# Kernel optimization log

Measured on AMD Instinct MI355X. Metric: run time of the kernel, lower is better.

Reference implementation:

```python
import jax, jax.numpy as jnp
import numpy as np

B, S, D = 30, 1024, 128      # batch (hardcoded by module), seq_len, input_dim
ET, H, NH = 128, 4, 128      # embed_time, num_heads, nhidden
DK = ET // H


def setup_inputs() -> dict:
    key = jax.random.key(0)
    ks = jax.random.split(key, 32)
    s = 0.05
    p = lambda i, shape: jax.random.normal(ks[i], shape, jnp.float32) * s
    return dict(
        x=jax.random.normal(ks[0], (B, S, D), jnp.float32),
        time_steps=jax.random.uniform(ks[1], (B, S), jnp.float32),
        # learned time embedding: Linear(1,1) and Linear(1, ET-1)
        w_lin=p(2, (1, 1)), b_lin=p(3, (1,)),
        w_per=p(4, (ET - 1, 1)), b_per=p(5, (ET - 1,)),
        # attention projections
        Wq=p(6, (ET, ET)), bq=p(7, (ET,)),
        Wk=p(8, (ET, ET)), bk=p(9, (ET,)),
        Wo=p(10, (NH, D * H)), bo=p(11, (NH,)),
        # bidirectional GRU (forward / backward directions)
        Wih_f=p(12, (3 * NH, NH)), Whh_f=p(13, (3 * NH, NH)),
        bih_f=p(14, (3 * NH,)), bhh_f=p(15, (3 * NH,)),
        Wih_b=p(16, (3 * NH, NH)), Whh_b=p(17, (3 * NH, NH)),
        bih_b=p(18, (3 * NH,)), bhh_b=p(19, (3 * NH,)),
        # classifier (no activations in original Sequential)
        W1=p(20, (128, 2 * NH)), b1=p(21, (128,)),
        W2=p(22, (64, 128)), b2=p(23, (64,)),
        W3=p(24, (6, 64)), b3=p(25, (6,)),
    )


def _gru_final(xseq, Wih, Whh, bih, bhh):
    # xseq: [S, B, NH]; returns final hidden [B, NH] (PyTorch GRU equations)
    def step(h, xt):
        gi = xt @ Wih.T + bih
        gh = h @ Whh.T + bhh
        ir, iz, inn = jnp.split(gi, 3, axis=-1)
        hr, hz, hn = jnp.split(gh, 3, axis=-1)
        r = jax.nn.sigmoid(ir + hr)
        z = jax.nn.sigmoid(iz + hz)
        n = jnp.tanh(inn + r * hn)
        h_new = (1.0 - z) * n + z * h
        return h_new, None
    h0 = jnp.zeros((xseq.shape[1], Whh.shape[1]), xseq.dtype)
    hT, _ = jax.lax.scan(step, h0, xseq)
    return hT


def reference(x, time_steps, w_lin, b_lin, w_per, b_per, Wq, bq, Wk, bk, Wo, bo,
              Wih_f, Whh_f, bih_f, bhh_f, Wih_b, Whh_b, bih_b, bhh_b,
              W1, b1, W2, b2, W3, b3):
    # learned time embedding: cat([Linear(1,1)(t), sin(Linear(1,ET-1)(t))], -1)
    tt = time_steps[..., None]                                   # [B,S,1]
    te = jnp.concatenate([tt @ w_lin.T + b_lin,
                          jnp.sin(tt @ w_per.T + b_per)], -1)    # [B,S,ET]
    # q/k projections, split into heads
    q = (te @ Wq.T + bq).reshape(B, S, H, DK).transpose(0, 2, 1, 3)  # [B,H,S,DK]
    k = (te @ Wk.T + bk).reshape(B, S, H, DK).transpose(0, 2, 1, 3)
    scores = jnp.einsum('bhqd,bhkd->bhqk', q, k) / jnp.sqrt(jnp.float32(DK))
    # mask=None, dropout=None => the repeat_interleave over the feature dim is
    # redundant: softmax over the key axis is identical for every feature, so
    # sum(p_attn * value) == softmax(scores) @ value exactly.
    attn = jax.nn.softmax(scores, axis=-1)                       # [B,H,S,S]
    ctx = jnp.einsum('bhqk,bkd->bhqd', attn, x)                  # [B,H,S,D]
    att_out = ctx.transpose(0, 2, 1, 3).reshape(B, S, H * D) @ Wo.T + bo  # [B,S,NH]
    # bidirectional GRU; only final hidden states are used downstream
    xs = att_out.transpose(1, 0, 2)                              # [S,B,NH]
    hf = _gru_final(xs, Wih_f, Whh_f, bih_f, bhh_f)
    hb = _gru_final(xs[::-1], Wih_b, Whh_b, bih_b, bhh_b)
    cin = jnp.concatenate([hf, hb], axis=-1)                     # [B,2*NH]
    h1 = cin @ W1.T + b1
    h2 = h1 @ W2.T + b2
    return h2 @ W3.T + b3                                        # [B,6]
```

## Files before the change

### kernel.cpp

```cpp
#include <hip/hip_runtime.h>
#include <math.h>

#define B_ 30
#define S_ 1024
#define D_ 128
#define ET_ 128
#define H_ 4
#define DK_ 32
#define NH_ 128
#define NPOS (B_*S_)

#define OFF_TE   0L
#define OFF_Q    3932160L
#define OFF_K    7864320L
#define OFF_CTX  11796480L
#define OFF_XS   0L
#define OFF_GIF  3932160L
#define OFF_GIB  15728640L
#define OFF_HF   27525120L
#define OFF_HB   27528960L

typedef __attribute__((ext_vector_type(4))) short short4v;
typedef __attribute__((ext_vector_type(8))) short short8v;
typedef __attribute__((ext_vector_type(4))) float f32x4;

__device__ __forceinline__ short f2bf(float x) {
    unsigned u = __builtin_bit_cast(unsigned, x);
    unsigned r = (u + 0x7FFFu + ((u >> 16) & 1u)) >> 16;
    return (short)r;
}
__device__ __forceinline__ float bf2f(short s) {
    unsigned u = ((unsigned)(unsigned short)s) << 16;
    return __builtin_bit_cast(float, u);
}

__device__ __forceinline__ short8v pack8(const float4 a, const float4 b) {
    short8v v;
    v[0]=f2bf(a.x); v[1]=f2bf(a.y); v[2]=f2bf(a.z); v[3]=f2bf(a.w);
    v[4]=f2bf(b.x); v[5]=f2bf(b.y); v[6]=f2bf(b.z); v[7]=f2bf(b.w);
    return v;
}

__device__ __forceinline__ void pack_hilo(const float4 a, const float4 b,
                                          short8v& hi, short8v& lo) {
    float v[8] = {a.x,a.y,a.z,a.w,b.x,b.y,b.z,b.w};
#pragma unroll
    for (int e = 0; e < 8; ++e) {
        hi[e] = f2bf(v[e]);
        lo[e] = f2bf(v[e] - bf2f(hi[e]));
    }
}

__device__ __forceinline__ float fsigmoid(float x) {
    return 1.f / (1.f + __expf(-x));
}
__device__ __forceinline__ float ftanh(float x) {
    return 1.f - 2.f / (__expf(2.f * x) + 1.f);
}

__device__ __forceinline__ void sync_lds() {
    asm volatile("s_waitcnt lgkmcnt(0)" ::: "memory");
    __builtin_amdgcn_sched_barrier(0);
    __builtin_amdgcn_s_barrier();
    __builtin_amdgcn_sched_barrier(0);
}

__global__ __launch_bounds__(256) void time_embed_kernel(
    const float* __restrict__ ts, const float* __restrict__ w_lin,
    const float* __restrict__ b_lin, const float* __restrict__ w_per,
    const float* __restrict__ b_per, float* __restrict__ te)
{
    const long idx = (long)blockIdx.x * 256 + threadIdx.x;
    const int pos = (int)(idx >> 7);
    const int j = (int)(idx & 127);
    const float tv = ts[pos];
    float v;
    if (j == 0) v = tv * w_lin[0] + b_lin[0];
    else        v = sinf(tv * w_per[j-1] + b_per[j-1]);
    te[idx] = v;
}

template<int REMAP, int FOLD>
__global__ __launch_bounds__(256) void gemm_mfma_kernel(
    const float* __restrict__ A, const float* __restrict__ W,
    const float* __restrict__ bias, const float* __restrict__ bias2,
    float* __restrict__ C, int M, int N, int K)
{
    __shared__ short A_hi[64][72], A_lo[64][72];
    __shared__ short W_hi[128][72], W_lo[128][72];
    const int t = threadIdx.x;
    const int m0 = blockIdx.x * 64;
    const int n0 = blockIdx.y * 128;
    const int w = t >> 6, lane = t & 63;
    const int l15 = lane & 15, lg = lane >> 4;

    f32x4 acc[8];
#pragma unroll
    for (int i = 0; i < 8; ++i) acc[i] = (f32x4){0.f,0.f,0.f,0.f};

    for (int k0 = 0; k0 < K; k0 += 64) {
        {
            const int r = t >> 2, c16 = (t & 3) * 16;
            const int m = m0 + r;
            long src;
            if (REMAP == 2) {
                const int s = m / B_, bb = m % B_;
                src = (long)((S_-1-s)*B_ + bb) * K;
            } else {
                src = (long)m * K;
            }
            const float4* ap = (const float4*)(A + src + k0 + c16);
            short8v h0, l0, h1, l1;
            pack_hilo(ap[0], ap[1], h0, l0);
            pack_hilo(ap[2], ap[3], h1, l1);
            *(short8v*)&A_hi[r][c16]     = h0;
            *(short8v*)&A_hi[r][c16 + 8] = h1;
            *(short8v*)&A_lo[r][c16]     = l0;
            *(short8v*)&A_lo[r][c16 + 8] = l1;
        }
        {
            const int n = t >> 1, c32 = (t & 1) * 32;
            const float4* wp = (const float4*)(W + (long)(n0 + n) * K + k0 + c32);
#pragma unroll
            for (int q = 0; q < 4; ++q) {
                short8v h, l;
                pack_hilo(wp[2*q], wp[2*q + 1], h, l);
                *(short8v*)&W_hi[n][c32 + 8*q] = h;
                *(short8v*)&W_lo[n][c32 + 8*q] = l;
            }
        }
        __syncthreads();
#pragma unroll
        for (int kk = 0; kk < 64; kk += 32) {
            short8v ah = *(const short8v*)&A_hi[16*w + l15][kk + 8*lg];
            short8v al = *(const short8v*)&A_lo[16*w + l15][kk + 8*lg];
#pragma unroll
            for (int nf = 0; nf < 8; ++nf) {
                short8v wh = *(const short8v*)&W_hi[16*nf + l15][kk + 8*lg];
                short8v wl = *(const short8v*)&W_lo[16*nf + l15][kk + 8*lg];
                acc[nf] = __builtin_amdgcn_mfma_f32_16x16x32_bf16(ah, wh, acc[nf], 0,0,0);
                acc[nf] = __builtin_amdgcn_mfma_f32_16x16x32_bf16(al, wh, acc[nf], 0,0,0);
                acc[nf] = __builtin_amdgcn_mfma_f32_16x16x32_bf16(ah, wl, acc[nf], 0,0,0);
            }
        }
        __syncthreads();
    }

#pragma unroll
    for (int nf = 0; nf < 8; ++nf) {
#pragma unroll
        for (int r = 0; r < 4; ++r) {
            const int n = n0 + 16*nf + l15;
            const int m = m0 + 16*w + 4*lg + r;
            float v = acc[nf][r] + bias[n];
            if (FOLD) { if (n < 256) v += bias2[n]; }
            if (REMAP == 1) {
                const int bb = m / S_, s = m % S_;
                C[(long)(s*B_ + bb) * N + n] = v;
            } else {
                C[(long)m * N + n] = v;
            }
        }
    }
}

#define SCALE_LOG2 (0.17677669529663687f * 1.4426950408889634f)

__global__ __launch_bounds__(256) void attn_kernel(
    const float* __restrict__ qbuf, const float* __restrict__ kbuf,
    const float* __restrict__ x, float* __restrict__ ctx)
{
    const int qt = blockIdx.x;
    const int h  = blockIdx.y;
    const int b  = blockIdx.z;
    const int q0 = qt * 64;
    const int t  = threadIdx.x;
    const int w    = t >> 6;
    const int lane = t & 63;
    const int l15  = lane & 15;
    const int lg   = lane >> 4;

    __shared__ short K_lds[64][40];
    __shared__ short XT_lds[128][68];
    __shared__ short P_lds[4][16][88];

    short8v qf;
    {
        const float* qp = qbuf + ((long)(b*S_ + q0 + 16*w + l15))*ET_ + h*DK_ + 8*lg;
        float4 a = *(const float4*)qp;
        float4 c = *(const float4*)(qp + 4);
        a.x*=SCALE_LOG2; a.y*=SCALE_LOG2; a.z*=SCALE_LOG2; a.w*=SCALE_LOG2;
        c.x*=SCALE_LOG2; c.y*=SCALE_LOG2; c.z*=SCALE_LOG2; c.w*=SCALE_LOG2;
        qf = pack8(a, c);
    }

    short8v ones;
#pragma unroll
    for (int i = 0; i < 8; ++i) ones[i] = (short)0x3F80;

    f32x4 acc[8];
#pragma unroll
    for (int i = 0; i < 8; ++i) acc[i] = (f32x4){0.f,0.f,0.f,0.f};
    float lsum = 0.f;
    const f32x4 zf = (f32x4){0.f,0.f,0.f,0.f};

    for (int kt = 0; kt < 16; ++kt) {
        const int key0 = kt * 64;
        {
            const int key = t >> 2, c8 = (t & 3) * 8;
            const float* kp = kbuf + ((long)(b*S_ + key0 + key))*ET_ + h*DK_ + c8;
            float4 a = *(const float4*)kp;
            float4 c = *(const float4*)(kp + 4);
            *(short8v*)&K_lds[key][c8] = pack8(a, c);
        }
        {
            const int k2 = t & 31;
            const int dg = t >> 5;
            const float* xp0 = x + ((long)(b*S_ + key0 + 2*k2))*D_ + 16*dg;
            const float* xp1 = xp0 + D_;
            float v0[16], v1[16];
#pragma unroll
            for (int j4 = 0; j4 < 4; ++j4) {
                float4 a = ((const float4*)xp0)[j4];
                float4 c = ((const float4*)xp1)[j4];
                v0[4*j4+0]=a.x; v0[4*j4+1]=a.y; v0[4*j4+2]=a.z; v0[4*j4+3]=a.w;
                v1[4*j4+0]=c.x; v1[4*j4+1]=c.y; v1[4*j4+2]=c.z; v1[4*j4+3]=c.w;
            }
#pragma unroll
            for (int j = 0; j < 16; ++j) {
                unsigned u = (unsigned)(unsigned short)f2bf(v0[j])
                           | ((unsigned)(unsigned short)f2bf(v1[j]) << 16);
                *(unsigned*)&XT_lds[16*dg + j][2*k2] = u;
            }
        }
        __syncthreads();

        f32x4 sc[4];
#pragma unroll
        for (int f = 0; f < 4; ++f) {
            short8v kf = *(const short8v*)&K_lds[16*f + l15][8*lg];
            sc[f] = __builtin_amdgcn_mfma_f32_16x16x32_bf16(kf, qf, zf, 0, 0, 0);
        }

        float pw[4][4];
        float ps = 0.f;
#pragma unroll
        for (int f = 0; f < 4; ++f)
#pragma unroll
            for (int r = 0; r < 4; ++r) {
                const float p = exp2f(sc[f][r]);
                ps += p;
                pw[f][r] = p - 1.f;
            }
        ps += __shfl_xor(ps, 16);
        ps += __shfl_xor(ps, 32);
        lsum += ps;

#pragma unroll
        for (int f = 0; f < 4; ++f) {
            unsigned lo = (unsigned)(unsigned short)f2bf(pw[f][0])
                        | ((unsigned)(unsigned short)f2bf(pw[f][1]) << 16);
            unsigned hi = (unsigned)(unsigned short)f2bf(pw[f][2])
                        | ((unsigned)(unsigned short)f2bf(pw[f][3]) << 16);
            *(unsigned*)&P_lds[w][l15][16*f + 4*lg]     = lo;
            *(unsigned*)&P_lds[w][l15][16*f + 4*lg + 2] = hi;
        }

#pragma unroll
        for (int kb = 0; kb < 2; ++kb) {
            short8v pa = *(const short8v*)&P_lds[w][l15][32*kb + 8*lg];
#pragma unroll
            for (int dq = 0; dq < 8; ++dq) {
                const short* xr = &XT_lds[16*dq + l15][32*kb + 8*lg];
                short4v lo = *(const short4v*)xr;
                short4v hi = *(const short4v*)(xr + 4);
                short8v xb = __builtin_shufflevector(lo, hi, 0,1,2,3,4,5,6,7);
                acc[dq] = __builtin_amdgcn_mfma_f32_16x16x32_bf16(ones, xb, acc[dq], 0, 0, 0);
                acc[dq] = __builtin_amdgcn_mfma_f32_16x16x32_bf16(pa,   xb, acc[dq], 0, 0, 0);
            }
        }
        __syncthreads();
    }

    const float inv = 1.f / lsum;
#pragma unroll
    for (int r = 0; r < 4; ++r) {
        const float ir = __shfl(inv, (lane & 48) | (4*lg + r));
        const long base = ((long)(b*S_ + q0 + 16*w + 4*lg + r)*H_ + h)*D_ + l15;
#pragma unroll
        for (int d = 0; d < 8; ++d)
            ctx[base + (long)d*16] = acc[d][r] * ir;
    }
}

__global__ __launch_bounds__(512, 1) void gru_kernel(
    const float* __restrict__ gi_f, const float* __restrict__ gi_b,
    const float* __restrict__ Whh_f, const float* __restrict__ bhh_f,
    const float* __restrict__ Whh_b, const float* __restrict__ bhh_b,
    float* __restrict__ hf, float* __restrict__ hb)
{
    const int bid = blockIdx.x;
    const int dir = bid / B_;
    const int b   = bid % B_;
    const float* gi  = dir ? gi_b  : gi_f;
    const float* Whh = dir ? Whh_b : Whh_f;
    const float* bhh = dir ? bhh_b : bhh_f;
    float* hout      = dir ? hb    : hf;
    const int t    = threadIdx.x;
    const int w    = t >> 6;
    const int lane = t & 63;
    const int l15  = lane & 15;
    const int lg   = lane >> 4;
    const int sel  = l15 >> 3;

    short8v wa[3][4];
#pragma unroll
    for (int rt = 0; rt < 3; ++rt) {
        const int row = (3*w + rt)*16 + l15;
#pragma unroll
        for (int kf = 0; kf < 4; ++kf) {
            const float* wp = Whh + (long)row*128 + 32*kf + 8*lg;
            float4 a = *(const float4*)wp;
            float4 c = *(const float4*)(wp + 4);
            wa[rt][kf] = pack8(a, c);
        }
    }

    __shared__ __align__(16) float ghs[800];
    __shared__ __align__(16) short hbf[2][2][160];

    float hreg = 0.f;
    float bnj = 0.f;
    float gar = 0.f, gaz = 0.f, gan = 0.f;
    float gbr = 0.f, gbz = 0.f, gbn = 0.f;
    if (t < 128) {
        hbf[0][0][t] = 0; hbf[0][1][t] = 0;
        bnj = bhh[256 + t];
        const float* g = gi + (long)b * 384;
        gar = g[t]; gaz = g[128+t]; gan = g[256+t];
    }
    __syncthreads();

#define GRU_STEP(CUR, GR, GZ, GN)                                              \
    {                                                                          \
        short8v hfrag[4];                                                      \
        _Pragma("unroll")                                                      \
        for (int kf = 0; kf < 4; ++kf)                                         \
            hfrag[kf] = *(const short8v*)&hbf[CUR][sel][32*kf + 8*lg];         \
        _Pragma("unroll")                                                      \
        for (int rt = 0; rt < 3; ++rt) {                                       \
            f32x4 cacc = (f32x4){0.f,0.f,0.f,0.f};                             \
            _Pragma("unroll")                                                  \
            for (int kf = 0; kf < 4; ++kf)                                     \
                cacc = __builtin_amdgcn_mfma_f32_16x16x32_bf16(                \
                    wa[rt][kf], hfrag[kf], cacc, 0,0,0);                       \
            if (l15 == 0)                                                      \
                *(f32x4*)&ghs[(3*w + rt)*16 + 4*lg] = cacc;                    \
            else if (l15 == 8)                                                 \
                *(f32x4*)&ghs[400 + (3*w + rt)*16 + 4*lg] = cacc;              \
        }                                                                      \
        sync_lds();                                                            \
        if (t < 128) {                                                         \
            const float ghr = ghs[t]       + ghs[400+t];                       \
            const float ghz = ghs[128+t]   + ghs[528+t];                       \
            const float ghn = ghs[256+t]   + ghs[656+t];                       \
            const float r = fsigmoid(GR + ghr);                                \
            const float z = fsigmoid(GZ + ghz);                                \
            const float n = ftanh (GN + r * (ghn + bnj));                      \
            hreg = (1.f - z)*n + z*hreg;                                       \
            const short hi = f2bf(hreg);                                       \
            hbf[(CUR)^1][0][t] = hi;                                           \
            hbf[(CUR)^1][1][t] = f2bf(hreg - bf2f(hi));                        \
        }                                                                      \
        sync_lds();                                                            \
    }

    for (int s = 0; s < S_; s += 2) {
        if (t < 128) {
            const float* g = gi + ((long)(s+1)*B_ + b) * 384;
            gbr = g[t]; gbz = g[128+t]; gbn = g[256+t];
        }
        GRU_STEP(0, gar, gaz, gan)
        if (t < 128 && s + 2 < S_) {
            const float* g = gi + ((long)(s+2)*B_ + b) * 384;
            gar = g[t]; gaz = g[128+t]; gan = g[256+t];
        }
        GRU_STEP(1, gbr, gbz, gbn)
    }
#undef GRU_STEP

    if (t < 128) hout[(long)b*128 + t] = hreg;
}

__global__ __launch_bounds__(128) void classifier_kernel(
    const float* __restrict__ hf, const float* __restrict__ hb,
    const float* __restrict__ W1, const float* __restrict__ b1,
    const float* __restrict__ W2, const float* __restrict__ b2,
    const float* __restrict__ W3, const float* __restrict__ b3,
    float* __restrict__ out)
{
    const int b = blockIdx.x;
    const int t = threadIdx.x;
    __shared__ float cin[256], a1[128], a2[64];
    cin[t]       = hf[(long)b*128 + t];
    cin[128 + t] = hb[(long)b*128 + t];
    __syncthreads();
    {
        float a = b1[t];
        for (int i = 0; i < 256; ++i) a = fmaf(W1[(long)t*256 + i], cin[i], a);
        a1[t] = a;
    }
    __syncthreads();
    if (t < 64) {
        float a = b2[t];
        for (int i = 0; i < 128; ++i) a = fmaf(W2[(long)t*128 + i], a1[i], a);
        a2[t] = a;
    }
    __syncthreads();
    if (t < 6) {
        float a = b3[t];
        for (int i = 0; i < 64; ++i) a = fmaf(W3[(long)t*64 + i], a2[i], a);
        out[(long)b*6 + t] = a;
    }
}

extern "C" void kernel_launch(void* const* d_in, const int* in_sizes, int n_in,
                              void* d_out, int out_size, void* d_ws, size_t ws_size,
                              hipStream_t stream)
{
    const float* x     = (const float*)d_in[0];
    const float* ts    = (const float*)d_in[1];
    const float* w_lin = (const float*)d_in[2];
    const float* b_lin = (const float*)d_in[3];
    const float* w_per = (const float*)d_in[4];
    const float* b_per = (const float*)d_in[5];
    const float* Wq    = (const float*)d_in[6];
    const float* bq    = (const float*)d_in[7];
    const float* Wk    = (const float*)d_in[8];
    const float* bk    = (const float*)d_in[9];
    const float* Wo    = (const float*)d_in[10];
    const float* bo    = (const float*)d_in[11];
    const float* Wih_f = (const float*)d_in[12];
    const float* Whh_f = (const float*)d_in[13];
    const float* bih_f = (const float*)d_in[14];
    const float* bhh_f = (const float*)d_in[15];
    const float* Wih_b = (const float*)d_in[16];
    const float* Whh_b = (const float*)d_in[17];
    const float* bih_b = (const float*)d_in[18];
    const float* bhh_b = (const float*)d_in[19];
    const float* W1    = (const float*)d_in[20];
    const float* b1    = (const float*)d_in[21];
    const float* W2    = (const float*)d_in[22];
    const float* b2    = (const float*)d_in[23];
    const float* W3    = (const float*)d_in[24];
    const float* b3    = (const float*)d_in[25];
    float* out = (float*)d_out;
    float* ws  = (float*)d_ws;

    float* te  = ws + OFF_TE;
    float* q   = ws + OFF_Q;
    float* k   = ws + OFF_K;
    float* ctx = ws + OFF_CTX;
    float* xs  = ws + OFF_XS;
    float* gif = ws + OFF_GIF;
    float* gib = ws + OFF_GIB;
    float* hf  = ws + OFF_HF;
    float* hb  = ws + OFF_HB;

    time_embed_kernel<<<NPOS*128/256, 256, 0, stream>>>(ts, w_lin, b_lin, w_per, b_per, te);
    gemm_mfma_kernel<0,0><<<dim3(NPOS/64, 1), 256, 0, stream>>>(te, Wq, bq, nullptr, q, NPOS, 128, 128);
    gemm_mfma_kernel<0,0><<<dim3(NPOS/64, 1), 256, 0, stream>>>(te, Wk, bk, nullptr, k, NPOS, 128, 128);
    attn_kernel<<<dim3(16, 4, 30), 256, 0, stream>>>(q, k, x, ctx);
    gemm_mfma_kernel<1,0><<<dim3(NPOS/64, 1), 256, 0, stream>>>(ctx, Wo, bo, nullptr, xs, NPOS, 128, 512);
    gemm_mfma_kernel<0,1><<<dim3(NPOS/64, 3), 256, 0, stream>>>(xs, Wih_f, bih_f, bhh_f, gif, NPOS, 384, 128);
    gemm_mfma_kernel<2,1><<<dim3(NPOS/64, 3), 256, 0, stream>>>(xs, Wih_b, bih_b, bhh_b, gib, NPOS, 384, 128);
    gru_kernel<<<60, 512, 0, stream>>>(gif, gib, Whh_f, bhh_f, Whh_b, bhh_b, hf, hb);
    classifier_kernel<<<30, 128, 0, stream>>>(hf, hb, W1, b1, W2, b2, W3, b3, out);
}
```

Baseline: 1.008 ms.

## Halve GRU block to 4 waves, split MFMA accumulation chains, prefetch two steps ahead

The sequential GRU kernel now runs 256 threads (4 waves), each wave holding 6 row tiles of Whh instead of 3. This is meant to cut barrier cost per recurrent step. Each tile's 4-deep MFMA accumulation is split into two independent chains that are summed at the end, which shortens the dependent MFMA latency. The gate-input prefetch is deepened to two steps ahead, with a 4-step unrolled loop. The trade-off is more MFMA work per wave each step and higher register pressure from the 24 weight fragments.

```diff
diff --git a/kernel.cpp b/kernel.cpp
--- a/kernel.cpp
+++ b/kernel.cpp
@@ -293,7 +293,7 @@
     }
 }
 
-__global__ __launch_bounds__(512, 1) void gru_kernel(
+__global__ __launch_bounds__(256, 1) void gru_kernel(
     const float* __restrict__ gi_f, const float* __restrict__ gi_b,
     const float* __restrict__ Whh_f, const float* __restrict__ bhh_f,
     const float* __restrict__ Whh_b, const float* __restrict__ bhh_b,
@@ -313,10 +313,10 @@
     const int lg   = lane >> 4;
     const int sel  = l15 >> 3;
 
-    short8v wa[3][4];
-#pragma unroll
-    for (int rt = 0; rt < 3; ++rt) {
-        const int row = (3*w + rt)*16 + l15;
+    short8v wa[6][4];
+#pragma unroll
+    for (int rt = 0; rt < 6; ++rt) {
+        const int row = (6*w + rt)*16 + l15;
 #pragma unroll
         for (int kf = 0; kf < 4; ++kf) {
             const float* wp = Whh + (long)row*128 + 32*kf + 8*lg;
@@ -333,13 +333,23 @@
     float bnj = 0.f;
     float gar = 0.f, gaz = 0.f, gan = 0.f;
     float gbr = 0.f, gbz = 0.f, gbn = 0.f;
+    float gcr = 0.f, gcz = 0.f, gcn = 0.f;
+    float gdr = 0.f, gdz = 0.f, gdn = 0.f;
     if (t < 128) {
         hbf[0][0][t] = 0; hbf[0][1][t] = 0;
         bnj = bhh[256 + t];
-        const float* g = gi + (long)b * 384;
-        gar = g[t]; gaz = g[128+t]; gan = g[256+t];
+        const float* g0 = gi + (long)b * 384;
+        gar = g0[t]; gaz = g0[128+t]; gan = g0[256+t];
+        const float* g1 = gi + ((long)B_ + b) * 384;
+        gbr = g1[t]; gbz = g1[128+t]; gbn = g1[256+t];
     }
     __syncthreads();
+
+#define LOADGI(R, Z, N, SS)                                                    \
+    if (t < 128 && (SS) < S_) {                                                \
+        const float* g = gi + ((long)(SS)*B_ + b) * 384;                       \
+        R = g[t]; Z = g[128+t]; N = g[256+t];                                  \
+    }
 
 #define GRU_STEP(CUR, GR, GZ, GN)                                              \
     {                                                                          \
@@ -348,16 +358,18 @@
         for (int kf = 0; kf < 4; ++kf)                                         \
             hfrag[kf] = *(const short8v*)&hbf[CUR][sel][32*kf + 8*lg];         \
         _Pragma("unroll")                                                      \
-        for (int rt = 0; rt < 3; ++rt) {                                       \
-            f32x4 cacc = (f32x4){0.f,0.f,0.f,0.f};                             \
-            _Pragma("unroll")                                                  \
-            for (int kf = 0; kf < 4; ++kf)                                     \
-                cacc = __builtin_amdgcn_mfma_f32_16x16x32_bf16(                \
-                    wa[rt][kf], hfrag[kf], cacc, 0,0,0);                       \
+        for (int rt = 0; rt < 6; ++rt) {                                       \
+            f32x4 ca = (f32x4){0.f,0.f,0.f,0.f};                               \
+            f32x4 cb = (f32x4){0.f,0.f,0.f,0.f};                               \
+            ca = __builtin_amdgcn_mfma_f32_16x16x32_bf16(wa[rt][0], hfrag[0], ca, 0,0,0); \
+            cb = __builtin_amdgcn_mfma_f32_16x16x32_bf16(wa[rt][2], hfrag[2], cb, 0,0,0); \
+            ca = __builtin_amdgcn_mfma_f32_16x16x32_bf16(wa[rt][1], hfrag[1], ca, 0,0,0); \
+            cb = __builtin_amdgcn_mfma_f32_16x16x32_bf16(wa[rt][3], hfrag[3], cb, 0,0,0); \
+            const f32x4 cc = ca + cb;                                          \
             if (l15 == 0)                                                      \
-                *(f32x4*)&ghs[(3*w + rt)*16 + 4*lg] = cacc;                    \
+                *(f32x4*)&ghs[(6*w + rt)*16 + 4*lg] = cc;                      \
             else if (l15 == 8)                                                 \
-                *(f32x4*)&ghs[400 + (3*w + rt)*16 + 4*lg] = cacc;              \
+                *(f32x4*)&ghs[400 + (6*w + rt)*16 + 4*lg] = cc;                \
         }                                                                      \
         sync_lds();                                                            \
         if (t < 128) {                                                         \
@@ -375,19 +387,18 @@
         sync_lds();                                                            \
     }
 
-    for (int s = 0; s < S_; s += 2) {
-        if (t < 128) {
-            const float* g = gi + ((long)(s+1)*B_ + b) * 384;
-            gbr = g[t]; gbz = g[128+t]; gbn = g[256+t];
-        }
+    for (int s = 0; s < S_; s += 4) {
+        LOADGI(gcr, gcz, gcn, s + 2)
         GRU_STEP(0, gar, gaz, gan)
-        if (t < 128 && s + 2 < S_) {
-            const float* g = gi + ((long)(s+2)*B_ + b) * 384;
-            gar = g[t]; gaz = g[128+t]; gan = g[256+t];
-        }
+        LOADGI(gdr, gdz, gdn, s + 3)
         GRU_STEP(1, gbr, gbz, gbn)
+        LOADGI(gar, gaz, gan, s + 4)
+        GRU_STEP(0, gcr, gcz, gcn)
+        LOADGI(gbr, gbz, gbn, s + 5)
+        GRU_STEP(1, gdr, gdz, gdn)
     }
 #undef GRU_STEP
+#undef LOADGI
 
     if (t < 128) hout[(long)b*128 + t] = hreg;
 }
@@ -474,6 +485,6 @@
     gemm_mfma_kernel<1,0><<<dim3(NPOS/64, 1), 256, 0, stream>>>(ctx, Wo, bo, nullptr, xs, NPOS, 128, 512);
     gemm_mfma_kernel<0,1><<<dim3(NPOS/64, 3), 256, 0, stream>>>(xs, Wih_f, bih_f, bhh_f, gif, NPOS, 384, 128);
     gemm_mfma_kernel<2,1><<<dim3(NPOS/64, 3), 256, 0, stream>>>(xs, Wih_b, bih_b, bhh_b, gib, NPOS, 384, 128);
-    gru_kernel<<<60, 512, 0, stream>>>(gif, gib, Whh_f, bhh_f, Whh_b, bhh_b, hf, hb);
+    gru_kernel<<<60, 256, 0, stream>>>(gif, gib, Whh_f, bhh_f, Whh_b, bhh_b, hf, hb);
     classifier_kernel<<<30, 128, 0, stream>>>(hf, hb, W1, b1, W2, b2, W3, b3, out);
 }
```

Measured after the change: 1.393 ms. 1.38x slower.

## Keep GRU gate math in registers and drop the per-step LDS round-trip

Applied to the files above, without the earlier changes.

The recurrent weight rows are reassigned so each wave owns the r, z and n gate rows for the same 16 hidden units. The hi/lo split-bf16 partial sums are now combined with a lane shuffle instead of being staged through shared memory. The gate nonlinearities are then computed in-register by lanes 0 and 16/32/48, which removes the ghs buffer and one of the two barriers per timestep on the serial critical path. The MFMA chain is also split into two independent accumulators to shorten dependency latency. In exchange, the elementwise gate work is concentrated on a few lanes per wave (4 units each), and the gi loads become vectorised float4 loads.

```diff
diff --git a/kernel.cpp b/kernel.cpp
--- a/kernel.cpp
+++ b/kernel.cpp
@@ -312,11 +312,12 @@
     const int l15  = lane & 15;
     const int lg   = lane >> 4;
     const int sel  = l15 >> 3;
+    const int j0   = 16*w + 4*lg;
 
     short8v wa[3][4];
 #pragma unroll
     for (int rt = 0; rt < 3; ++rt) {
-        const int row = (3*w + rt)*16 + l15;
+        const int row = 128*rt + 16*w + l15;
 #pragma unroll
         for (int kf = 0; kf < 4; ++kf) {
             const float* wp = Whh + (long)row*128 + 32*kf + 8*lg;
@@ -326,20 +327,30 @@
         }
     }
 
-    __shared__ __align__(16) float ghs[800];
+    const f32x4 bn = *(const f32x4*)(bhh + 256 + j0);
+
     __shared__ __align__(16) short hbf[2][2][160];
-
-    float hreg = 0.f;
-    float bnj = 0.f;
-    float gar = 0.f, gaz = 0.f, gan = 0.f;
-    float gbr = 0.f, gbz = 0.f, gbn = 0.f;
-    if (t < 128) {
-        hbf[0][0][t] = 0; hbf[0][1][t] = 0;
-        bnj = bhh[256 + t];
+    if (t < 128) { hbf[0][0][t] = 0; hbf[0][1][t] = 0; }
+
+    f32x4 hcur = (f32x4){0.f,0.f,0.f,0.f};
+
+    f32x4 gar = {0,0,0,0}, gaz = {0,0,0,0}, gan = {0,0,0,0};
+    f32x4 gbr = {0,0,0,0}, gbz = {0,0,0,0}, gbn = {0,0,0,0};
+    if (l15 == 0) {
         const float* g = gi + (long)b * 384;
-        gar = g[t]; gaz = g[128+t]; gan = g[256+t];
+        gar = *(const f32x4*)(g + j0);
+        gaz = *(const f32x4*)(g + 128 + j0);
+        gan = *(const f32x4*)(g + 256 + j0);
     }
     __syncthreads();
+
+#define LOADGI(R, Z, N, SS)                                                    \
+    if (l15 == 0 && (SS) < S_) {                                               \
+        const float* g = gi + ((long)(SS)*B_ + b) * 384;                       \
+        R = *(const f32x4*)(g + j0);                                           \
+        Z = *(const f32x4*)(g + 128 + j0);                                     \
+        N = *(const f32x4*)(g + 256 + j0);                                     \
+    }
 
 #define GRU_STEP(CUR, GR, GZ, GN)                                              \
     {                                                                          \
@@ -347,49 +358,49 @@
         _Pragma("unroll")                                                      \
         for (int kf = 0; kf < 4; ++kf)                                         \
             hfrag[kf] = *(const short8v*)&hbf[CUR][sel][32*kf + 8*lg];         \
+        f32x4 gh[3];                                                           \
         _Pragma("unroll")                                                      \
         for (int rt = 0; rt < 3; ++rt) {                                       \
-            f32x4 cacc = (f32x4){0.f,0.f,0.f,0.f};                             \
+            f32x4 ca = (f32x4){0.f,0.f,0.f,0.f};                               \
+            f32x4 cb = (f32x4){0.f,0.f,0.f,0.f};                               \
+            ca = __builtin_amdgcn_mfma_f32_16x16x32_bf16(wa[rt][0], hfrag[0], ca, 0,0,0); \
+            cb = __builtin_amdgcn_mfma_f32_16x16x32_bf16(wa[rt][2], hfrag[2], cb, 0,0,0); \
+            ca = __builtin_amdgcn_mfma_f32_16x16x32_bf16(wa[rt][1], hfrag[1], ca, 0,0,0); \
+            cb = __builtin_amdgcn_mfma_f32_16x16x32_bf16(wa[rt][3], hfrag[3], cb, 0,0,0); \
+            f32x4 cc = ca + cb;                                                \
             _Pragma("unroll")                                                  \
-            for (int kf = 0; kf < 4; ++kf)                                     \
-                cacc = __builtin_amdgcn_mfma_f32_16x16x32_bf16(                \
-                    wa[rt][kf], hfrag[kf], cacc, 0,0,0);                       \
-            if (l15 == 0)                                                      \
-                *(f32x4*)&ghs[(3*w + rt)*16 + 4*lg] = cacc;                    \
-            else if (l15 == 8)                                                 \
-                *(f32x4*)&ghs[400 + (3*w + rt)*16 + 4*lg] = cacc;              \
+            for (int r = 0; r < 4; ++r) cc[r] += __shfl_xor(cc[r], 8);         \
+            gh[rt] = cc;                                                       \
+        }                                                                      \
+        if (l15 == 0) {                                                        \
+            short4v hv_hi, hv_lo;                                              \
+            _Pragma("unroll")                                                  \
+            for (int r = 0; r < 4; ++r) {                                      \
+                const float rr = fsigmoid(GR[r] + gh[0][r]);                   \
+                const float zz = fsigmoid(GZ[r] + gh[1][r]);                   \
+                const float nn = ftanh (GN[r] + rr * (gh[2][r] + bn[r]));      \
+                hcur[r] = (1.f - zz)*nn + zz*hcur[r];                          \
+                const short hi = f2bf(hcur[r]);                                \
+                hv_hi[r] = hi;                                                 \
+                hv_lo[r] = f2bf(hcur[r] - bf2f(hi));                           \
+            }                                                                  \
+            *(short4v*)&hbf[(CUR)^1][0][j0] = hv_hi;                           \
+            *(short4v*)&hbf[(CUR)^1][1][j0] = hv_lo;                           \
         }                                                                      \
         sync_lds();                                                            \
-        if (t < 128) {                                                         \
-            const float ghr = ghs[t]       + ghs[400+t];                       \
-            const float ghz = ghs[128+t]   + ghs[528+t];                       \
-            const float ghn = ghs[256+t]   + ghs[656+t];                       \
-            const float r = fsigmoid(GR + ghr);                                \
-            const float z = fsigmoid(GZ + ghz);                                \
-            const float n = ftanh (GN + r * (ghn + bnj));                      \
-            hreg = (1.f - z)*n + z*hreg;                                       \
-            const short hi = f2bf(hreg);                                       \
-            hbf[(CUR)^1][0][t] = hi;                                           \
-            hbf[(CUR)^1][1][t] = f2bf(hreg - bf2f(hi));                        \
-        }                                                                      \
-        sync_lds();                                                            \
     }
 
     for (int s = 0; s < S_; s += 2) {
-        if (t < 128) {
-            const float* g = gi + ((long)(s+1)*B_ + b) * 384;
-            gbr = g[t]; gbz = g[128+t]; gbn = g[256+t];
-        }
+        LOADGI(gbr, gbz, gbn, s + 1)
         GRU_STEP(0, gar, gaz, gan)
-        if (t < 128 && s + 2 < S_) {
-            const float* g = gi + ((long)(s+2)*B_ + b) * 384;
-            gar = g[t]; gaz = g[128+t]; gan = g[256+t];
-        }
+        LOADGI(gar, gaz, gan, s + 2)
         GRU_STEP(1, gbr, gbz, gbn)
     }
 #undef GRU_STEP
-
-    if (t < 128) hout[(long)b*128 + t] = hreg;
+#undef LOADGI
+
+    if (l15 == 0)
+        *(f32x4*)&hout[(long)b*128 + j0] = hcur;
 }
 
 __global__ __launch_bounds__(128) void classifier_kernel(
```

Result: slower. 3.634 ms (+260.7%).

## Compute GRU gate update redundantly per wave to drop second barrier

Applied to the files above, without the earlier changes.

In the GRU recurrence kernel, every wave now computes the full 128-element gate update and hidden state itself (two elements per lane) and writes into its own private copy of the bf16 hidden-state buffer. The gh scratch buffer is double-buffered by step parity. Together these remove the second block-wide barrier per time step, since no wave has to wait for another wave's hidden-state writes. The cost is redundant transcendental math and gi loads across all waves, plus more LDS use.

```diff
diff --git a/kernel.cpp b/kernel.cpp
--- a/kernel.cpp
+++ b/kernel.cpp
@@ -312,6 +312,8 @@
     const int l15  = lane & 15;
     const int lg   = lane >> 4;
     const int sel  = l15 >> 3;
+    const int j0   = lane;
+    const int j1   = 64 + lane;
 
     short8v wa[3][4];
 #pragma unroll
@@ -326,27 +328,39 @@
         }
     }
 
-    __shared__ __align__(16) float ghs[800];
-    __shared__ __align__(16) short hbf[2][2][160];
-
-    float hreg = 0.f;
-    float bnj = 0.f;
-    float gar = 0.f, gaz = 0.f, gan = 0.f;
-    float gbr = 0.f, gbz = 0.f, gbn = 0.f;
-    if (t < 128) {
-        hbf[0][0][t] = 0; hbf[0][1][t] = 0;
-        bnj = bhh[256 + t];
+    __shared__ __align__(16) float ghs[2][800];
+    __shared__ __align__(16) short hbf[8][2][2][160];
+
+    const float bn0 = bhh[256 + j0];
+    const float bn1 = bhh[256 + j1];
+
+    float h0 = 0.f, h1 = 0.f;
+
+    hbf[w][0][0][j0] = 0; hbf[w][0][0][j1] = 0;
+    hbf[w][0][1][j0] = 0; hbf[w][0][1][j1] = 0;
+
+    float gar0=0.f, gaz0=0.f, gan0=0.f, gar1=0.f, gaz1=0.f, gan1=0.f;
+    float gbr0=0.f, gbz0=0.f, gbn0=0.f, gbr1=0.f, gbz1=0.f, gbn1=0.f;
+    {
         const float* g = gi + (long)b * 384;
-        gar = g[t]; gaz = g[128+t]; gan = g[256+t];
+        gar0 = g[j0]; gaz0 = g[128+j0]; gan0 = g[256+j0];
+        gar1 = g[j1]; gaz1 = g[128+j1]; gan1 = g[256+j1];
     }
     __syncthreads();
 
-#define GRU_STEP(CUR, GR, GZ, GN)                                              \
+#define LOADGI(R0,Z0,N0,R1,Z1,N1, SS)                                          \
+    if ((SS) < S_) {                                                           \
+        const float* g = gi + ((long)(SS)*B_ + b) * 384;                       \
+        R0 = g[j0]; Z0 = g[128+j0]; N0 = g[256+j0];                            \
+        R1 = g[j1]; Z1 = g[128+j1]; N1 = g[256+j1];                            \
+    }
+
+#define GRU_STEP(CUR, GR0,GZ0,GN0, GR1,GZ1,GN1)                                \
     {                                                                          \
         short8v hfrag[4];                                                      \
         _Pragma("unroll")                                                      \
         for (int kf = 0; kf < 4; ++kf)                                         \
-            hfrag[kf] = *(const short8v*)&hbf[CUR][sel][32*kf + 8*lg];         \
+            hfrag[kf] = *(const short8v*)&hbf[w][CUR][sel][32*kf + 8*lg];      \
         _Pragma("unroll")                                                      \
         for (int rt = 0; rt < 3; ++rt) {                                       \
             f32x4 cacc = (f32x4){0.f,0.f,0.f,0.f};                             \
@@ -355,41 +369,48 @@
                 cacc = __builtin_amdgcn_mfma_f32_16x16x32_bf16(                \
                     wa[rt][kf], hfrag[kf], cacc, 0,0,0);                       \
             if (l15 == 0)                                                      \
-                *(f32x4*)&ghs[(3*w + rt)*16 + 4*lg] = cacc;                    \
+                *(f32x4*)&ghs[CUR][(3*w + rt)*16 + 4*lg] = cacc;               \
             else if (l15 == 8)                                                 \
-                *(f32x4*)&ghs[400 + (3*w + rt)*16 + 4*lg] = cacc;              \
+                *(f32x4*)&ghs[CUR][400 + (3*w + rt)*16 + 4*lg] = cacc;         \
         }                                                                      \
         sync_lds();                                                            \
-        if (t < 128) {                                                         \
-            const float ghr = ghs[t]       + ghs[400+t];                       \
-            const float ghz = ghs[128+t]   + ghs[528+t];                       \
-            const float ghn = ghs[256+t]   + ghs[656+t];                       \
-            const float r = fsigmoid(GR + ghr);                                \
-            const float z = fsigmoid(GZ + ghz);                                \
-            const float n = ftanh (GN + r * (ghn + bnj));                      \
-            hreg = (1.f - z)*n + z*hreg;                                       \
-            const short hi = f2bf(hreg);                                       \
-            hbf[(CUR)^1][0][t] = hi;                                           \
-            hbf[(CUR)^1][1][t] = f2bf(hreg - bf2f(hi));                        \
+        {                                                                      \
+            const float ghr0 = ghs[CUR][j0]     + ghs[CUR][400+j0];            \
+            const float ghz0 = ghs[CUR][128+j0] + ghs[CUR][528+j0];            \
+            const float ghn0 = ghs[CUR][256+j0] + ghs[CUR][656+j0];            \
+            const float ghr1 = ghs[CUR][j1]     + ghs[CUR][400+j1];            \
+            const float ghz1 = ghs[CUR][128+j1] + ghs[CUR][528+j1];            \
+            const float ghn1 = ghs[CUR][256+j1] + ghs[CUR][656+j1];            \
+            const float r0 = fsigmoid(GR0 + ghr0);                             \
+            const float z0 = fsigmoid(GZ0 + ghz0);                             \
+            const float n0 = ftanh (GN0 + r0 * (ghn0 + bn0));                  \
+            h0 = (1.f - z0)*n0 + z0*h0;                                        \
+            const float r1 = fsigmoid(GR1 + ghr1);                             \
+            const float z1 = fsigmoid(GZ1 + ghz1);                             \
+            const float n1 = ftanh (GN1 + r1 * (ghn1 + bn1));                  \
+            h1 = (1.f - z1)*n1 + z1*h1;                                        \
+            const short hi0 = f2bf(h0);                                        \
+            const short hi1 = f2bf(h1);                                        \
+            hbf[w][(CUR)^1][0][j0] = hi0;                                      \
+            hbf[w][(CUR)^1][0][j1] = hi1;                                      \
+            hbf[w][(CUR)^1][1][j0] = f2bf(h0 - bf2f(hi0));                     \
+            hbf[w][(CUR)^1][1][j1] = f2bf(h1 - bf2f(hi1));                     \
         }                                                                      \
-        sync_lds();                                                            \
     }
 
     for (int s = 0; s < S_; s += 2) {
-        if (t < 128) {
-            const float* g = gi + ((long)(s+1)*B_ + b) * 384;
-            gbr = g[t]; gbz = g[128+t]; gbn = g[256+t];
-        }
-        GRU_STEP(0, gar, gaz, gan)
-        if (t < 128 && s + 2 < S_) {
-            const float* g = gi + ((long)(s+2)*B_ + b) * 384;
-            gar = g[t]; gaz = g[128+t]; gan = g[256+t];
-        }
-        GRU_STEP(1, gbr, gbz, gbn)
+        LOADGI(gbr0,gbz0,gbn0, gbr1,gbz1,gbn1, s + 1)
+        GRU_STEP(0, gar0,gaz0,gan0, gar1,gaz1,gan1)
+        LOADGI(gar0,gaz0,gan0, gar1,gaz1,gan1, s + 2)
+        GRU_STEP(1, gbr0,gbz0,gbn0, gbr1,gbz1,gbn1)
     }
 #undef GRU_STEP
-
-    if (t < 128) hout[(long)b*128 + t] = hreg;
+#undef LOADGI
+
+    if (w == 0) {
+        hout[(long)b*128 + j0] = h0;
+        hout[(long)b*128 + j1] = h1;
+    }
 }
 
 __global__ __launch_bounds__(128) void classifier_kernel(
```

After: 1.298 ms. 28.8% more time.
